# Performance work log

Hardware: AMD Instinct MI355X
Metric: run time of the kernel (lower is better)

The kernel has to match this reference:

```python
import jax, jax.numpy as jnp
import numpy as np

N, E, G = 50000, 800000, 500          # nodes, edges, graphs
NFEAT, NHID, EFEAT = 128, 128, 16
L, NCLASS = 4, 10
BN_EPS = 1e-5


def setup_inputs() -> dict:
    key = jax.random.key(0)
    ks = jax.random.split(key, 10)
    w = lambda k, shape: (jax.random.normal(k, shape, jnp.float32) * 0.05)
    return {
        "h": jax.random.normal(ks[0], (N, NFEAT), jnp.float32),
        "edge_attr": jax.random.normal(ks[1], (E, EFEAT), jnp.float32),
        "edge_index": jax.random.randint(ks[2], (2, E), 0, N),
        "edge_feat_mat": jnp.zeros((1,), jnp.int32),   # placeholder (unused by simplified conv)
        "pair_info": jnp.zeros((1,), jnp.int32),       # placeholder (unused by simplified conv)
        "batch": jnp.sort(jax.random.randint(ks[3], (N,), 0, G)),
        "emb_W": w(ks[4], (NFEAT, NHID)), "emb_b": jnp.zeros((NHID,), jnp.float32),
        "conv_W": w(ks[5], (L, NHID, NHID)), "conv_b": jnp.zeros((L, NHID), jnp.float32),
        "conv_We": w(ks[6], (L, EFEAT, NHID)), "conv_be": jnp.zeros((L, NHID), jnp.float32),
        "bn_gamma": jnp.ones((L, NHID), jnp.float32), "bn_beta": jnp.zeros((L, NHID), jnp.float32),
        "jk_W": w(ks[7], (L + 1, NHID, NCLASS)), "jk_b": jnp.zeros((L + 1, NCLASS), jnp.float32),
    }


def _conv(h, edge_attr, src, dst, W, b, We, be):
    # GIN-style message passing: gather src features, add projected edge feats,
    # scatter-add into dst, then a dense transform of (self + aggregate).
    msg = h[src] + edge_attr @ We + be                      # [E, NHID]
    agg = jax.ops.segment_sum(msg, dst, num_segments=h.shape[0])  # [N, NHID]
    return (h + agg) @ W + b


def _batch_norm(x, gamma, beta):
    mu = jnp.mean(x, axis=0)
    var = jnp.mean(jnp.square(x - mu), axis=0)  # biased, as in torch BN training
    return (x - mu) * jax.lax.rsqrt(var + BN_EPS) * gamma + beta


def reference(h, edge_attr, edge_index, edge_feat_mat, pair_info, batch,
              emb_W, emb_b, conv_W, conv_b, conv_We, conv_be,
              bn_gamma, bn_beta, jk_W, jk_b):
    src, dst = edge_index[0], edge_index[1]
    h = h @ emb_W + emb_b                                   # embedding_h
    h_list = [h]
    for layer in range(L):
        z = _conv(h, edge_attr, src, dst,
                  conv_W[layer], conv_b[layer], conv_We[layer], conv_be[layer])
        z = _batch_norm(z, bn_gamma[layer], bn_beta[layer])
        z = jax.nn.relu(z)
        h = z + h_list[layer]                               # residual (dropout p=0)
        h_list.append(h)
    # JK: sum of per-layer linear heads applied to global_add_pool
    out = jnp.zeros((G, NCLASS), jnp.float32)
    for layer in range(L + 1):
        pooled = jax.ops.segment_sum(h_list[layer], batch, num_segments=G)  # [G, NHID]
        out = out + pooled @ jk_W[layer] + jk_b[layer]
    return out
```

## Files before the change

### kernel.cpp

```cpp
#include <hip/hip_runtime.h>

#define NH 128
#define LAYERS 4
#define BW 128
#define CHUNK 4096

typedef __attribute__((ext_vector_type(8))) short short8;
typedef __attribute__((ext_vector_type(4))) float f32x4;

__device__ __forceinline__ unsigned short f2bf(float f) {
    unsigned u = __float_as_uint(f);
    u += 0x7fffu + ((u >> 16) & 1u);
    return (unsigned short)(u >> 16);
}
__device__ __forceinline__ float bflo(unsigned u) { return __uint_as_float(u << 16); }
__device__ __forceinline__ float bfhi(unsigned u) { return __uint_as_float(u & 0xffff0000u); }
__device__ __forceinline__ unsigned packbf(float x, float y) {
    return (unsigned)f2bf(x) | ((unsigned)f2bf(y) << 16);
}

__global__ void wswz_kernel(const float* __restrict__ emb_W, const float* __restrict__ conv_W,
                            unsigned short* __restrict__ Wsw) {
    int idx = blockIdx.x * 256 + threadIdx.x;
    if (idx >= 5 * 8192) return;
    int m = idx >> 13, i = idx & 8191;
    const float* W = (m == 0) ? emb_W : conv_W + (size_t)(m - 1) * 16384;
    float2 w2 = ((const float2*)W)[i];
    int k = i >> 6, n = (i & 63) * 2;
    int kc = k >> 5, quad = (k >> 3) & 3, j = k & 7;
    int base = m * 16384 + (((n >> 4) * 4 + kc) * 4 + quad) * 128 + j;
    Wsw[base + ((n & 15) << 3)] = f2bf(w2.x);
    Wsw[base + (((n + 1) & 15) << 3)] = f2bf(w2.y);
}

__global__ __launch_bounds__(256) void bhist_kernel(const int* __restrict__ dst, int E,
                                                    int* __restrict__ gH, int NBKT, int NCH,
                                                    const int* __restrict__ batch,
                                                    int* __restrict__ gstart, int N, int G) {
    __shared__ int hist[512];
    int b = blockIdx.x, t = threadIdx.x;
    for (int i = t; i < NBKT; i += 256) hist[i] = 0;
    __syncthreads();
    int base = b * CHUNK, end = min(base + CHUNK, E);
    for (int e = base + t; e < end; e += 256)
        atomicAdd(&hist[dst[e] >> 7], 1);
    __syncthreads();
    for (int i = t; i < NBKT; i += 256) gH[i * NCH + b] = hist[i];

    for (int i = b * 256 + t; i < N; i += gridDim.x * 256) {
        int bb = batch[i];
        int prev = (i == 0) ? -1 : batch[i - 1];
        for (int g = prev + 1; g <= bb; ++g) gstart[g] = i;
        if (i == N - 1)
            for (int g = bb + 1; g <= G; ++g) gstart[g] = N;
    }
}

__global__ __launch_bounds__(256) void block_sum_kernel(const int* __restrict__ deg,
                                                        int* __restrict__ bsum, int n) {
    __shared__ int red[256];
    int t = threadIdx.x;
    int base = blockIdx.x * 1024;
    int s = 0;
#pragma unroll
    for (int i = 0; i < 4; ++i) {
        int idx = base + i * 256 + t;
        if (idx < n) s += deg[idx];
    }
    red[t] = s;
    __syncthreads();
    for (int off = 128; off > 0; off >>= 1) {
        if (t < off) red[t] += red[t + off];
        __syncthreads();
    }
    if (t == 0) bsum[blockIdx.x] = red[0];
}

__global__ __launch_bounds__(1024) void scan_partials_kernel(int* __restrict__ bsum, int nb,
                                                             int* __restrict__ total_out, int n) {
    __shared__ int part[1024];
    int t = threadIdx.x;
    int v = (t < nb) ? bsum[t] : 0;
    part[t] = v;
    __syncthreads();
    for (int off = 1; off < 1024; off <<= 1) {
        int u = (t >= off) ? part[t - off] : 0;
        __syncthreads();
        part[t] += u;
        __syncthreads();
    }
    if (t < nb) bsum[t] = part[t] - v;
    if (t == 1023) total_out[n] = part[1023];
}

__global__ __launch_bounds__(256) void local_scan_kernel(const int* __restrict__ deg,
                                                         const int* __restrict__ bsum,
                                                         int* __restrict__ outA, int n) {
    __shared__ int part[256];
    int t = threadIdx.x;
    int base = blockIdx.x * 1024 + t * 4;
    int v0 = 0, v1 = 0, v2 = 0, v3 = 0;
    if (base + 3 < n) {
        int4 v = *(const int4*)(deg + base);
        v0 = v.x; v1 = v.y; v2 = v.z; v3 = v.w;
    } else {
        if (base + 0 < n) v0 = deg[base + 0];
        if (base + 1 < n) v1 = deg[base + 1];
        if (base + 2 < n) v2 = deg[base + 2];
        if (base + 3 < n) v3 = deg[base + 3];
    }
    int tsum = v0 + v1 + v2 + v3;
    part[t] = tsum;
    __syncthreads();
    for (int off = 1; off < 256; off <<= 1) {
        int u = (t >= off) ? part[t - off] : 0;
        __syncthreads();
        part[t] += u;
        __syncthreads();
    }
    int run = bsum[blockIdx.x] + part[t] - tsum;
    int r0 = run, r1 = run + v0, r2 = r1 + v1, r3 = r2 + v2;
    if (base + 3 < n) {
        *(int4*)(outA + base) = make_int4(r0, r1, r2, r3);
    } else {
        if (base + 0 < n) outA[base + 0] = r0;
        if (base + 1 < n) outA[base + 1] = r1;
        if (base + 2 < n) outA[base + 2] = r2;
        if (base + 3 < n) outA[base + 3] = r3;
    }
}

__global__ __launch_bounds__(256) void bplace_kernel(const int* __restrict__ src,
                                                     const int* __restrict__ dst, int E,
                                                     const int* __restrict__ gOff,
                                                     int NBKT, int NCH,
                                                     int2* __restrict__ bkt) {
    __shared__ int cur[512];
    int b = blockIdx.x, t = threadIdx.x;
    for (int i = t; i < NBKT; i += 256) cur[i] = gOff[i * NCH + b];
    __syncthreads();
    int base = b * CHUNK, end = min(base + CHUNK, E);
    for (int e = base + t; e < end; e += 256) {
        int d = dst[e];
        int p = atomicAdd(&cur[d >> 7], 1);
        bkt[p] = make_int2(src[e], ((d & (BW - 1)) << 25) | e);
    }
}

__global__ __launch_bounds__(256) void bfinal_kernel(const int2* __restrict__ bkt,
                                                     const int* __restrict__ gOff, int NCH,
                                                     int* __restrict__ row_start,
                                                     int2* __restrict__ pk,
                                                     int N, int E) {
    __shared__ int cnt[BW], par[BW];
    int b = blockIdx.x, t = threadIdx.x;
    int s = gOff[b * NCH];
    int e = (b + 1 < (int)gridDim.x) ? gOff[(b + 1) * NCH] : E;
    if (t < BW) cnt[t] = 0;
    __syncthreads();
    for (int p = s + t; p < e; p += 256)
        atomicAdd(&cnt[(unsigned)bkt[p].y >> 25], 1);
    __syncthreads();
    if (t < BW) par[t] = cnt[t];
    __syncthreads();
    for (int off = 1; off < BW; off <<= 1) {
        int u = (t < BW && t >= off) ? par[t - off] : 0;
        __syncthreads();
        if (t < BW) par[t] += u;
        __syncthreads();
    }
    int node = b * BW + t;
    if (t < BW) {
        int excl = par[t] - cnt[t];
        if (node <= N) row_start[node] = s + excl;
        cnt[t] = s + excl;
    }
    if (b == 0 && t == 0) row_start[N] = E;
    __syncthreads();
    for (int p = s + t; p < e; p += 256) {
        int2 v = bkt[p];
        int dloc = (unsigned)v.y >> 25;
        int pos = atomicAdd(&cnt[dloc], 1);
        pk[pos] = make_int2(v.x, v.y & 0x1FFFFFF);
    }
}

__global__ __launch_bounds__(256) void easum_kernel(const float* __restrict__ edge_attr,
                                                    const int2* __restrict__ pk,
                                                    const int* __restrict__ row_start,
                                                    float* __restrict__ easum, int N) {
    int t = threadIdx.x;
    int node = blockIdx.x * 16 + (t >> 4);
    int k = t & 15;
    if (node >= N) return;
    int rs = row_start[node], re = row_start[node + 1];
    float acc = 0.f;
    for (int p = rs; p < re; ++p)
        acc += edge_attr[(size_t)pk[p].y * 16 + k];
    easum[node * 16 + k] = acc;
}

__global__ __launch_bounds__(256) void aggregate_kernel(
    const unsigned* __restrict__ hbfu, const int2* __restrict__ pk,
    const int* __restrict__ row_start, const float* __restrict__ easum,
    const float* __restrict__ We, const float* __restrict__ be,
    unsigned* __restrict__ xbfu, int N) {
    __shared__ float2 WeL[16 * 64];
    int t = threadIdx.x;
    const float2* Wg2 = (const float2*)We;
    for (int i = t; i < 16 * 64; i += 256) WeL[i] = Wg2[i];
    __syncthreads();

    int wave = t >> 6, lane = t & 63;
    int n = blockIdx.x * 4 + wave;
    if (n >= N) return;
    unsigned uself = hbfu[(size_t)n * 64 + lane];
    float2 acc = make_float2(bflo(uself), bfhi(uself));
    float2 acc2 = make_float2(0.f, 0.f);
    float2 acc3 = make_float2(0.f, 0.f);
    float2 acc4 = make_float2(0.f, 0.f);
    int rs = row_start[n], re = row_start[n + 1];
    float myea = (lane < 16) ? easum[n * 16 + lane] : 0.f;

    for (int base = rs; base < re; base += 64) {
        int cnt = min(64, re - base);
        int myS = (base + lane < re) ? pk[base + lane].x : 0;
        int j = 0;
        for (; j + 15 < cnt; j += 16) {
            int s0 = __shfl(myS, j);      int s1 = __shfl(myS, j + 1);
            int s2 = __shfl(myS, j + 2);  int s3 = __shfl(myS, j + 3);
            int s4 = __shfl(myS, j + 4);  int s5 = __shfl(myS, j + 5);
            int s6 = __shfl(myS, j + 6);  int s7 = __shfl(myS, j + 7);
            int s8 = __shfl(myS, j + 8);  int s9 = __shfl(myS, j + 9);
            int sa = __shfl(myS, j + 10); int sb = __shfl(myS, j + 11);
            int sc = __shfl(myS, j + 12); int sd = __shfl(myS, j + 13);
            int se = __shfl(myS, j + 14); int sf = __shfl(myS, j + 15);
            unsigned u0 = hbfu[(size_t)s0 * 64 + lane];
            unsigned u1 = hbfu[(size_t)s1 * 64 + lane];
            unsigned u2 = hbfu[(size_t)s2 * 64 + lane];
            unsigned u3 = hbfu[(size_t)s3 * 64 + lane];
            unsigned u4 = hbfu[(size_t)s4 * 64 + lane];
            unsigned u5 = hbfu[(size_t)s5 * 64 + lane];
            unsigned u6 = hbfu[(size_t)s6 * 64 + lane];
            unsigned u7 = hbfu[(size_t)s7 * 64 + lane];
            unsigned u8 = hbfu[(size_t)s8 * 64 + lane];
            unsigned u9 = hbfu[(size_t)s9 * 64 + lane];
            unsigned ua = hbfu[(size_t)sa * 64 + lane];
            unsigned ub = hbfu[(size_t)sb * 64 + lane];
            unsigned uc = hbfu[(size_t)sc * 64 + lane];
            unsigned ud = hbfu[(size_t)sd * 64 + lane];
            unsigned ue = hbfu[(size_t)se * 64 + lane];
            unsigned uf = hbfu[(size_t)sf * 64 + lane];
            acc.x  += bflo(u0) + bflo(u1) + bflo(u2) + bflo(u3);
            acc.y  += bfhi(u0) + bfhi(u1) + bfhi(u2) + bfhi(u3);
            acc2.x += bflo(u4) + bflo(u5) + bflo(u6) + bflo(u7);
            acc2.y += bfhi(u4) + bfhi(u5) + bfhi(u6) + bfhi(u7);
            acc3.x += bflo(u8) + bflo(u9) + bflo(ua) + bflo(ub);
            acc3.y += bfhi(u8) + bfhi(u9) + bfhi(ua) + bfhi(ub);
            acc4.x += bflo(uc) + bflo(ud) + bflo(ue) + bflo(uf);
            acc4.y += bfhi(uc) + bfhi(ud) + bfhi(ue) + bfhi(uf);
        }
        for (; j + 3 < cnt; j += 4) {
            int s0 = __shfl(myS, j);
            int s1 = __shfl(myS, j + 1);
            int s2 = __shfl(myS, j + 2);
            int s3 = __shfl(myS, j + 3);
            unsigned u0 = hbfu[(size_t)s0 * 64 + lane];
            unsigned u1 = hbfu[(size_t)s1 * 64 + lane];
            unsigned u2 = hbfu[(size_t)s2 * 64 + lane];
            unsigned u3 = hbfu[(size_t)s3 * 64 + lane];
            acc.x += bflo(u0) + bflo(u1) + bflo(u2) + bflo(u3);
            acc.y += bfhi(u0) + bfhi(u1) + bfhi(u2) + bfhi(u3);
        }
        for (; j < cnt; ++j) {
            int s = __shfl(myS, j);
            unsigned u = hbfu[(size_t)s * 64 + lane];
            acc.x += bflo(u);
            acc.y += bfhi(u);
        }
    }
    acc.x += (acc2.x + acc3.x) + acc4.x;
    acc.y += (acc2.y + acc3.y) + acc4.y;

    float degf = (float)(re - rs);
    float2 be2 = ((const float2*)be)[lane];
#pragma unroll
    for (int k = 0; k < 16; ++k) {
        float e = __shfl(myea, k);
        float2 w = WeL[k * 64 + lane];
        acc.x = fmaf(e, w.x, acc.x);
        acc.y = fmaf(e, w.y, acc.y);
    }
    acc.x += degf * be2.x;
    acc.y += degf * be2.y;
    xbfu[(size_t)n * 64 + lane] = packbf(acc.x, acc.y);
}

__global__ __launch_bounds__(256) void gemm_mfma_kernel(
    const unsigned short* __restrict__ Abf, const float* __restrict__ Af32,
    const unsigned short* __restrict__ Wsw, const float* __restrict__ bias,
    unsigned short* __restrict__ Zbf,
    int N, float* __restrict__ bnsum, float* __restrict__ bnsumsq) {
    __shared__ unsigned short Wl[128 * 128];
    __shared__ float bnL[2 * NH];
    int t = threadIdx.x;
    {
        const float4* Wg = (const float4*)Wsw;
        float4* Wl4 = (float4*)Wl;
        for (int i = t; i < 2048; i += 256) Wl4[i] = Wg[i];
    }
    if (t < 2 * NH) bnL[t] = 0.f;
    __syncthreads();

    int wave = t >> 6, lane = t & 63;
    int quad = lane >> 4, ln = lane & 15;
    int row0 = blockIdx.x * 128 + wave * 32;

    f32x4 acc[2][8];
#pragma unroll
    for (int nt = 0; nt < 8; ++nt) {
        float bv = bias[nt * 16 + ln];
        acc[0][nt] = (f32x4){bv, bv, bv, bv};
        acc[1][nt] = (f32x4){bv, bv, bv, bv};
    }

    for (int kc = 0; kc < 4; ++kc) {
        short8 afr[2];
        if (Af32) {
#pragma unroll
            for (int mt = 0; mt < 2; ++mt) {
                int ar = row0 + mt * 16 + ln; if (ar >= N) ar = N - 1;
                const float4* ap = (const float4*)(Af32 + (size_t)ar * NH + kc * 32 + quad * 8);
                float4 a0 = ap[0], a1 = ap[1];
                short8 v;
                v[0] = (short)f2bf(a0.x); v[1] = (short)f2bf(a0.y);
                v[2] = (short)f2bf(a0.z); v[3] = (short)f2bf(a0.w);
                v[4] = (short)f2bf(a1.x); v[5] = (short)f2bf(a1.y);
                v[6] = (short)f2bf(a1.z); v[7] = (short)f2bf(a1.w);
                afr[mt] = v;
            }
        } else {
#pragma unroll
            for (int mt = 0; mt < 2; ++mt) {
                int ar = row0 + mt * 16 + ln; if (ar >= N) ar = N - 1;
                afr[mt] = *(const short8*)(Abf + (size_t)ar * NH + kc * 32 + quad * 8);
            }
        }
#pragma unroll
        for (int nt = 0; nt < 8; ++nt) {
            short8 bfr = *(const short8*)(Wl + ((nt * 4 + kc) * 4 + quad) * 128 + ln * 8);
            acc[0][nt] = __builtin_amdgcn_mfma_f32_16x16x32_bf16(afr[0], bfr, acc[0][nt], 0, 0, 0);
            acc[1][nt] = __builtin_amdgcn_mfma_f32_16x16x32_bf16(afr[1], bfr, acc[1][nt], 0, 0, 0);
        }
    }

#pragma unroll
    for (int mt = 0; mt < 2; ++mt)
#pragma unroll
        for (int r = 0; r < 4; ++r) {
            int row = row0 + mt * 16 + quad * 4 + r;
            if (row < N) {
#pragma unroll
                for (int nt = 0; nt < 8; ++nt)
                    Zbf[(size_t)row * NH + nt * 16 + ln] = f2bf(acc[mt][nt][r]);
            }
        }

    if (bnsum) {
#pragma unroll
        for (int nt = 0; nt < 8; ++nt) {
            float s = 0.f, q = 0.f;
#pragma unroll
            for (int mt = 0; mt < 2; ++mt)
#pragma unroll
                for (int r = 0; r < 4; ++r) {
                    int row = row0 + mt * 16 + quad * 4 + r;
                    if (row < N) { float v = acc[mt][nt][r]; s += v; q += v * v; }
                }
            s += __shfl_xor(s, 16); s += __shfl_xor(s, 32);
            q += __shfl_xor(q, 16); q += __shfl_xor(q, 32);
            if (quad == 0) {
                atomicAdd(&bnL[nt * 16 + ln], s);
                atomicAdd(&bnL[NH + nt * 16 + ln], q);
            }
        }
        __syncthreads();
        if (t < NH) {
            atomicAdd(&bnsum[t], bnL[t]);
            atomicAdd(&bnsumsq[t], bnL[NH + t]);
        }
    }
}

__global__ __launch_bounds__(256) void update_pool_kernel(
    const unsigned* __restrict__ zbfu, unsigned* __restrict__ hbfu,
    const float* __restrict__ bnsum, const float* __restrict__ bnsumsq,
    const float* __restrict__ gamma, const float* __restrict__ beta,
    float invN, const int* __restrict__ gstart, float* __restrict__ pooled) {
    int g = blockIdx.x, t = threadIdx.x;
    __shared__ float scL[NH], shL[NH];
    __shared__ float2 red[256];
    if (t < NH) {
        float mu = bnsum[t] * invN;
        float var = fmaf(bnsumsq[t], invN, -mu * mu);
        float sc = gamma[t] * rsqrtf(var + 1e-5f);
        scL[t] = sc;
        shL[t] = beta[t] - mu * sc;
    }
    __syncthreads();
    int s = gstart[g], e = gstart[g + 1];
    int c2 = t & 63, half = t >> 6;
    float2 sc = make_float2(scL[2 * c2], scL[2 * c2 + 1]);
    float2 sh = make_float2(shL[2 * c2], shL[2 * c2 + 1]);
    float2 pacc = make_float2(0.f, 0.f);
    for (int n = s + half; n < e; n += 4) {
        size_t i = (size_t)n * 64 + c2;
        unsigned zu = zbfu[i];
        unsigned hu = hbfu[i];
        float rx = fmaxf(fmaf(bflo(zu), sc.x, sh.x), 0.f) + bflo(hu);
        float ry = fmaxf(fmaf(bfhi(zu), sc.y, sh.y), 0.f) + bfhi(hu);
        hbfu[i] = packbf(rx, ry);
        pacc.x += rx; pacc.y += ry;
    }
    red[t] = pacc;
    __syncthreads();
    if (t < 64) {
        float2 a = red[t], b = red[t + 64], c = red[t + 128], d = red[t + 192];
        ((float2*)pooled)[(size_t)g * 64 + c2] =
            make_float2((a.x + b.x) + (c.x + d.x), (a.y + b.y) + (c.y + d.y));
    }
}

__global__ __launch_bounds__(256) void pool_kernel(
    const unsigned* __restrict__ hbfu, const int* __restrict__ gstart,
    float* __restrict__ pooled, int G) {
    int g = blockIdx.x, t = threadIdx.x;
    __shared__ float2 red[256];
    int s = gstart[g], e = gstart[g + 1];
    int c2 = t & 63, half = t >> 6;
    float2 pacc = make_float2(0.f, 0.f);
    for (int n = s + half; n < e; n += 4) {
        unsigned u = hbfu[(size_t)n * 64 + c2];
        pacc.x += bflo(u);
        pacc.y += bfhi(u);
    }
    red[t] = pacc;
    __syncthreads();
    if (t < 64) {
        float2 a = red[t], b = red[t + 64], c = red[t + 128], d = red[t + 192];
        ((float2*)pooled)[(size_t)g * 64 + c2] =
            make_float2((a.x + b.x) + (c.x + d.x), (a.y + b.y) + (c.y + d.y));
    }
}

__global__ void jk_kernel(const float* __restrict__ pooled, const float* __restrict__ jkW,
                          const float* __restrict__ jkb, float* __restrict__ out, int G) {
    int idx = blockIdx.x * blockDim.x + threadIdx.x;
    if (idx >= G * 10) return;
    int g = idx / 10, c = idx % 10;
    float acc = 0.f;
    for (int l = 0; l < LAYERS + 1; ++l) {
        acc += jkb[l * 10 + c];
        const float* pg = pooled + ((size_t)l * G + g) * NH;
        const float* wl = jkW + (size_t)l * NH * 10 + c;
        float s = 0.f;
#pragma unroll 16
        for (int k = 0; k < NH; ++k) s = fmaf(pg[k], wl[k * 10], s);
        acc += s;
    }
    out[idx] = acc;
}

extern "C" void kernel_launch(void* const* d_in, const int* in_sizes, int n_in,
                              void* d_out, int out_size, void* d_ws, size_t ws_size,
                              hipStream_t stream) {
    const float* h_in      = (const float*)d_in[0];
    const float* edge_attr = (const float*)d_in[1];
    const int*   edge_idx  = (const int*)d_in[2];
    const int*   batch     = (const int*)d_in[5];
    const float* emb_W     = (const float*)d_in[6];
    const float* emb_b     = (const float*)d_in[7];
    const float* conv_W    = (const float*)d_in[8];
    const float* conv_b    = (const float*)d_in[9];
    const float* conv_We   = (const float*)d_in[10];
    const float* conv_be   = (const float*)d_in[11];
    const float* bn_gamma  = (const float*)d_in[12];
    const float* bn_beta   = (const float*)d_in[13];
    const float* jk_W      = (const float*)d_in[14];
    const float* jk_b      = (const float*)d_in[15];
    float* out = (float*)d_out;

    const int N = in_sizes[0] / NH;
    const int E = in_sizes[1] / 16;
    const int G = out_size / 10;
    const int NBKT = (N + BW - 1) / BW;
    const int NCH  = (E + CHUNK - 1) / CHUNK;
    const int NTOT = NBKT * NCH;
    const int NBW  = (NTOT + 1023) / 1024;

    const int* src = edge_idx;
    const int* dst = edge_idx + E;

    size_t off = 0;
    auto alloc = [&](size_t bytes) -> void* {
        void* p = (char*)d_ws + off;
        off += (bytes + 255) & ~(size_t)255;
        return p;
    };
    unsigned short* hbf = (unsigned short*)alloc((size_t)N * NH * 2);
    unsigned short* xbf = (unsigned short*)alloc((size_t)N * NH * 2);
    unsigned short* zbf = (unsigned short*)alloc((size_t)N * NH * 2);
    unsigned short* Wsw = (unsigned short*)alloc((size_t)5 * NH * NH * 2);
    float* pooled  = (float*)alloc((size_t)(LAYERS + 1) * G * NH * 4);
    float* easum   = (float*)alloc((size_t)N * 16 * 4);
    size_t zero_off = off;
    float* bnsum   = (float*)alloc((size_t)LAYERS * NH * 4);
    float* bnsumsq = (float*)alloc((size_t)LAYERS * NH * 4);
    size_t zero_bytes = off - zero_off;
    int* gH        = (int*)alloc((size_t)(NTOT + 1) * 4);
    int* bsumW     = (int*)alloc((size_t)NBW * 4);
    int* gstart    = (int*)alloc((size_t)(G + 1) * 4);
    int* row_start = (int*)alloc((size_t)(N + 1) * 4);
    int2* bkt      = (int2*)alloc((size_t)E * 8);
    int2* pk       = (int2*)alloc((size_t)E * 8);
    (void)ws_size; (void)n_in;

    hipMemsetAsync((char*)d_ws + zero_off, 0, zero_bytes, stream);

    wswz_kernel<<<(5 * 8192 + 255) / 256, 256, 0, stream>>>(emb_W, conv_W, Wsw);

    bhist_kernel<<<NCH, 256, 0, stream>>>(dst, E, gH, NBKT, NCH, batch, gstart, N, G);
    block_sum_kernel<<<NBW, 256, 0, stream>>>(gH, bsumW, NTOT);
    scan_partials_kernel<<<1, 1024, 0, stream>>>(bsumW, NBW, gH, NTOT);
    local_scan_kernel<<<NBW, 256, 0, stream>>>(gH, bsumW, gH, NTOT);
    bplace_kernel<<<NCH, 256, 0, stream>>>(src, dst, E, gH, NBKT, NCH, bkt);
    bfinal_kernel<<<NBKT, 256, 0, stream>>>(bkt, gH, NCH, row_start, pk, N, E);
    easum_kernel<<<(N + 15) / 16, 256, 0, stream>>>(edge_attr, pk, row_start, easum, N);

    dim3 gemm_grid((N + 127) / 128);
    dim3 agg_grid((N + 3) / 4);

    gemm_mfma_kernel<<<gemm_grid, 256, 0, stream>>>(
        nullptr, h_in, Wsw, emb_b, hbf, N, nullptr, nullptr);
    pool_kernel<<<G, 256, 0, stream>>>((const unsigned*)hbf, gstart, pooled, G);

    for (int l = 0; l < LAYERS; ++l) {
        aggregate_kernel<<<agg_grid, 256, 0, stream>>>(
            (const unsigned*)hbf, pk, row_start, easum,
            conv_We + (size_t)l * 16 * NH, conv_be + (size_t)l * NH,
            (unsigned*)xbf, N);
        gemm_mfma_kernel<<<gemm_grid, 256, 0, stream>>>(
            xbf, nullptr, Wsw + (size_t)(l + 1) * NH * NH, conv_b + (size_t)l * NH,
            zbf, N, bnsum + (size_t)l * NH, bnsumsq + (size_t)l * NH);
        update_pool_kernel<<<G, 256, 0, stream>>>(
            (const unsigned*)zbf, (unsigned*)hbf,
            bnsum + (size_t)l * NH, bnsumsq + (size_t)l * NH,
            bn_gamma + (size_t)l * NH, bn_beta + (size_t)l * NH,
            1.0f / (float)N, gstart, pooled + (size_t)(l + 1) * G * NH);
    }

    jk_kernel<<<(G * 10 + 255) / 256, 256, 0, stream>>>(pooled, jk_W, jk_b, out, G);
}
```

Baseline: 549.1 us.

## Fuse neighbor aggregation with MFMA GEMM and BN statistics per node tile

Replaces the separate aggregate and GEMM kernels in each layer with one kernel. Each 512-thread block aggregates a 128-node tile into swizzled LDS, then runs the bf16 MFMA transform on it and accumulates the BatchNorm sums. This removes the xbf intermediate round trip through global memory and one launch per layer. In exchange the grid drops to one block per 128 nodes, each wave walks 16 nodes one after another, and the weights are read from global memory instead of LDS. That may reduce how well the latency-bound gather is hidden.

```diff
diff --git a/kernel.cpp b/kernel.cpp
--- a/kernel.cpp
+++ b/kernel.cpp
@@ -200,116 +200,173 @@
     easum[node * 16 + k] = acc;
 }
 
-__global__ __launch_bounds__(256) void aggregate_kernel(
+__global__ __launch_bounds__(512) void agg_gemm_kernel(
     const unsigned* __restrict__ hbfu, const int2* __restrict__ pk,
     const int* __restrict__ row_start, const float* __restrict__ easum,
     const float* __restrict__ We, const float* __restrict__ be,
-    unsigned* __restrict__ xbfu, int N) {
+    const unsigned short* __restrict__ Wsw, const float* __restrict__ bias,
+    unsigned short* __restrict__ Zbf, int N,
+    float* __restrict__ bnsum, float* __restrict__ bnsumsq) {
+    __shared__ unsigned xL[128 * 64];
     __shared__ float2 WeL[16 * 64];
+    __shared__ float bnL[2 * NH];
     int t = threadIdx.x;
     const float2* Wg2 = (const float2*)We;
-    for (int i = t; i < 16 * 64; i += 256) WeL[i] = Wg2[i];
+    for (int i = t; i < 16 * 64; i += 512) WeL[i] = Wg2[i];
+    if (t < 2 * NH) bnL[t] = 0.f;
     __syncthreads();
 
     int wave = t >> 6, lane = t & 63;
-    int n = blockIdx.x * 4 + wave;
-    if (n >= N) return;
-    unsigned uself = hbfu[(size_t)n * 64 + lane];
-    float2 acc = make_float2(bflo(uself), bfhi(uself));
-    float2 acc2 = make_float2(0.f, 0.f);
-    float2 acc3 = make_float2(0.f, 0.f);
-    float2 acc4 = make_float2(0.f, 0.f);
-    int rs = row_start[n], re = row_start[n + 1];
-    float myea = (lane < 16) ? easum[n * 16 + lane] : 0.f;
-
-    for (int base = rs; base < re; base += 64) {
-        int cnt = min(64, re - base);
-        int myS = (base + lane < re) ? pk[base + lane].x : 0;
-        int j = 0;
-        for (; j + 15 < cnt; j += 16) {
-            int s0 = __shfl(myS, j);      int s1 = __shfl(myS, j + 1);
-            int s2 = __shfl(myS, j + 2);  int s3 = __shfl(myS, j + 3);
-            int s4 = __shfl(myS, j + 4);  int s5 = __shfl(myS, j + 5);
-            int s6 = __shfl(myS, j + 6);  int s7 = __shfl(myS, j + 7);
-            int s8 = __shfl(myS, j + 8);  int s9 = __shfl(myS, j + 9);
-            int sa = __shfl(myS, j + 10); int sb = __shfl(myS, j + 11);
-            int sc = __shfl(myS, j + 12); int sd = __shfl(myS, j + 13);
-            int se = __shfl(myS, j + 14); int sf = __shfl(myS, j + 15);
-            unsigned u0 = hbfu[(size_t)s0 * 64 + lane];
-            unsigned u1 = hbfu[(size_t)s1 * 64 + lane];
-            unsigned u2 = hbfu[(size_t)s2 * 64 + lane];
-            unsigned u3 = hbfu[(size_t)s3 * 64 + lane];
-            unsigned u4 = hbfu[(size_t)s4 * 64 + lane];
-            unsigned u5 = hbfu[(size_t)s5 * 64 + lane];
-            unsigned u6 = hbfu[(size_t)s6 * 64 + lane];
-            unsigned u7 = hbfu[(size_t)s7 * 64 + lane];
-            unsigned u8 = hbfu[(size_t)s8 * 64 + lane];
-            unsigned u9 = hbfu[(size_t)s9 * 64 + lane];
-            unsigned ua = hbfu[(size_t)sa * 64 + lane];
-            unsigned ub = hbfu[(size_t)sb * 64 + lane];
-            unsigned uc = hbfu[(size_t)sc * 64 + lane];
-            unsigned ud = hbfu[(size_t)sd * 64 + lane];
-            unsigned ue = hbfu[(size_t)se * 64 + lane];
-            unsigned uf = hbfu[(size_t)sf * 64 + lane];
-            acc.x  += bflo(u0) + bflo(u1) + bflo(u2) + bflo(u3);
-            acc.y  += bfhi(u0) + bfhi(u1) + bfhi(u2) + bfhi(u3);
-            acc2.x += bflo(u4) + bflo(u5) + bflo(u6) + bflo(u7);
-            acc2.y += bfhi(u4) + bfhi(u5) + bfhi(u6) + bfhi(u7);
-            acc3.x += bflo(u8) + bflo(u9) + bflo(ua) + bflo(ub);
-            acc3.y += bfhi(u8) + bfhi(u9) + bfhi(ua) + bfhi(ub);
-            acc4.x += bflo(uc) + bflo(ud) + bflo(ue) + bflo(uf);
-            acc4.y += bfhi(uc) + bfhi(ud) + bfhi(ue) + bfhi(uf);
-        }
-        for (; j + 3 < cnt; j += 4) {
-            int s0 = __shfl(myS, j);
-            int s1 = __shfl(myS, j + 1);
-            int s2 = __shfl(myS, j + 2);
-            int s3 = __shfl(myS, j + 3);
-            unsigned u0 = hbfu[(size_t)s0 * 64 + lane];
-            unsigned u1 = hbfu[(size_t)s1 * 64 + lane];
-            unsigned u2 = hbfu[(size_t)s2 * 64 + lane];
-            unsigned u3 = hbfu[(size_t)s3 * 64 + lane];
-            acc.x += bflo(u0) + bflo(u1) + bflo(u2) + bflo(u3);
-            acc.y += bfhi(u0) + bfhi(u1) + bfhi(u2) + bfhi(u3);
-        }
-        for (; j < cnt; ++j) {
-            int s = __shfl(myS, j);
-            unsigned u = hbfu[(size_t)s * 64 + lane];
-            acc.x += bflo(u);
-            acc.y += bfhi(u);
-        }
-    }
-    acc.x += (acc2.x + acc3.x) + acc4.x;
-    acc.y += (acc2.y + acc3.y) + acc4.y;
-
-    float degf = (float)(re - rs);
-    float2 be2 = ((const float2*)be)[lane];
-#pragma unroll
-    for (int k = 0; k < 16; ++k) {
-        float e = __shfl(myea, k);
-        float2 w = WeL[k * 64 + lane];
-        acc.x = fmaf(e, w.x, acc.x);
-        acc.y = fmaf(e, w.y, acc.y);
-    }
-    acc.x += degf * be2.x;
-    acc.y += degf * be2.y;
-    xbfu[(size_t)n * 64 + lane] = packbf(acc.x, acc.y);
+    int b = blockIdx.x;
+
+    for (int i = 0; i < 16; ++i) {
+        int nl = wave * 16 + i;
+        int n = b * BW + nl;
+        unsigned widx = nl * 64 + (lane ^ ((nl & 15) << 2));
+        if (n >= N) { xL[widx] = 0u; continue; }
+        unsigned uself = hbfu[(size_t)n * 64 + lane];
+        float2 acc = make_float2(bflo(uself), bfhi(uself));
+        float2 acc2 = make_float2(0.f, 0.f);
+        float2 acc3 = make_float2(0.f, 0.f);
+        float2 acc4 = make_float2(0.f, 0.f);
+        int rs = row_start[n], re = row_start[n + 1];
+        float myea = (lane < 16) ? easum[n * 16 + lane] : 0.f;
+
+        for (int base = rs; base < re; base += 64) {
+            int cnt = min(64, re - base);
+            int myS = (base + lane < re) ? pk[base + lane].x : 0;
+            int j = 0;
+            for (; j + 15 < cnt; j += 16) {
+                int s0 = __shfl(myS, j);      int s1 = __shfl(myS, j + 1);
+                int s2 = __shfl(myS, j + 2);  int s3 = __shfl(myS, j + 3);
+                int s4 = __shfl(myS, j + 4);  int s5 = __shfl(myS, j + 5);
+                int s6 = __shfl(myS, j + 6);  int s7 = __shfl(myS, j + 7);
+                int s8 = __shfl(myS, j + 8);  int s9 = __shfl(myS, j + 9);
+                int sa = __shfl(myS, j + 10); int sb = __shfl(myS, j + 11);
+                int sc = __shfl(myS, j + 12); int sd = __shfl(myS, j + 13);
+                int se = __shfl(myS, j + 14); int sf = __shfl(myS, j + 15);
+                unsigned u0 = hbfu[(size_t)s0 * 64 + lane];
+                unsigned u1 = hbfu[(size_t)s1 * 64 + lane];
+                unsigned u2 = hbfu[(size_t)s2 * 64 + lane];
+                unsigned u3 = hbfu[(size_t)s3 * 64 + lane];
+                unsigned u4 = hbfu[(size_t)s4 * 64 + lane];
+                unsigned u5 = hbfu[(size_t)s5 * 64 + lane];
+                unsigned u6 = hbfu[(size_t)s6 * 64 + lane];
+                unsigned u7 = hbfu[(size_t)s7 * 64 + lane];
+                unsigned u8 = hbfu[(size_t)s8 * 64 + lane];
+                unsigned u9 = hbfu[(size_t)s9 * 64 + lane];
+                unsigned ua = hbfu[(size_t)sa * 64 + lane];
+                unsigned ub = hbfu[(size_t)sb * 64 + lane];
+                unsigned uc = hbfu[(size_t)sc * 64 + lane];
+                unsigned ud = hbfu[(size_t)sd * 64 + lane];
+                unsigned ue = hbfu[(size_t)se * 64 + lane];
+                unsigned uf = hbfu[(size_t)sf * 64 + lane];
+                acc.x  += bflo(u0) + bflo(u1) + bflo(u2) + bflo(u3);
+                acc.y  += bfhi(u0) + bfhi(u1) + bfhi(u2) + bfhi(u3);
+                acc2.x += bflo(u4) + bflo(u5) + bflo(u6) + bflo(u7);
+                acc2.y += bfhi(u4) + bfhi(u5) + bfhi(u6) + bfhi(u7);
+                acc3.x += bflo(u8) + bflo(u9) + bflo(ua) + bflo(ub);
+                acc3.y += bfhi(u8) + bfhi(u9) + bfhi(ua) + bfhi(ub);
+                acc4.x += bflo(uc) + bflo(ud) + bflo(ue) + bflo(uf);
+                acc4.y += bfhi(uc) + bfhi(ud) + bfhi(ue) + bfhi(uf);
+            }
+            for (; j + 3 < cnt; j += 4) {
+                int s0 = __shfl(myS, j);
+                int s1 = __shfl(myS, j + 1);
+                int s2 = __shfl(myS, j + 2);
+                int s3 = __shfl(myS, j + 3);
+                unsigned u0 = hbfu[(size_t)s0 * 64 + lane];
+                unsigned u1 = hbfu[(size_t)s1 * 64 + lane];
+                unsigned u2 = hbfu[(size_t)s2 * 64 + lane];
+                unsigned u3 = hbfu[(size_t)s3 * 64 + lane];
+                acc.x += bflo(u0) + bflo(u1) + bflo(u2) + bflo(u3);
+                acc.y += bfhi(u0) + bfhi(u1) + bfhi(u2) + bfhi(u3);
+            }
+            for (; j < cnt; ++j) {
+                int s = __shfl(myS, j);
+                unsigned u = hbfu[(size_t)s * 64 + lane];
+                acc.x += bflo(u);
+                acc.y += bfhi(u);
+            }
+        }
+        acc.x += (acc2.x + acc3.x) + acc4.x;
+        acc.y += (acc2.y + acc3.y) + acc4.y;
+
+        float degf = (float)(re - rs);
+        float2 be2 = ((const float2*)be)[lane];
+#pragma unroll
+        for (int k = 0; k < 16; ++k) {
+            float e = __shfl(myea, k);
+            float2 w = WeL[k * 64 + lane];
+            acc.x = fmaf(e, w.x, acc.x);
+            acc.y = fmaf(e, w.y, acc.y);
+        }
+        acc.x += degf * be2.x;
+        acc.y += degf * be2.y;
+        xL[widx] = packbf(acc.x, acc.y);
+    }
+
+    int quad = lane >> 4, ln = lane & 15;
+    int ar = wave * 16 + ln;
+    f32x4 acc[8];
+#pragma unroll
+    for (int nt = 0; nt < 8; ++nt) {
+        float bv = bias[nt * 16 + ln];
+        acc[nt] = (f32x4){bv, bv, bv, bv};
+    }
+#pragma unroll
+    for (int kc = 0; kc < 4; ++kc) {
+        int widx = ar * 64 + ((kc * 16 + quad * 4) ^ ((ar & 15) << 2));
+        short8 afr = *(const short8*)(xL + widx);
+#pragma unroll
+        for (int nt = 0; nt < 8; ++nt) {
+            short8 bfr = *(const short8*)(Wsw + ((nt * 4 + kc) * 4 + quad) * 128 + ln * 8);
+            acc[nt] = __builtin_amdgcn_mfma_f32_16x16x32_bf16(afr, bfr, acc[nt], 0, 0, 0);
+        }
+    }
+
+#pragma unroll
+    for (int r = 0; r < 4; ++r) {
+        int row = b * BW + wave * 16 + quad * 4 + r;
+        if (row < N) {
+#pragma unroll
+            for (int nt = 0; nt < 8; ++nt)
+                Zbf[(size_t)row * NH + nt * 16 + ln] = f2bf(acc[nt][r]);
+        }
+    }
+
+#pragma unroll
+    for (int nt = 0; nt < 8; ++nt) {
+        float s = 0.f, q = 0.f;
+#pragma unroll
+        for (int r = 0; r < 4; ++r) {
+            int row = b * BW + wave * 16 + quad * 4 + r;
+            if (row < N) { float v = acc[nt][r]; s += v; q += v * v; }
+        }
+        s += __shfl_xor(s, 16); s += __shfl_xor(s, 32);
+        q += __shfl_xor(q, 16); q += __shfl_xor(q, 32);
+        if (quad == 0) {
+            atomicAdd(&bnL[nt * 16 + ln], s);
+            atomicAdd(&bnL[NH + nt * 16 + ln], q);
+        }
+    }
+    __syncthreads();
+    if (t < NH) {
+        atomicAdd(&bnsum[t], bnL[t]);
+        atomicAdd(&bnsumsq[t], bnL[NH + t]);
+    }
 }
 
 __global__ __launch_bounds__(256) void gemm_mfma_kernel(
-    const unsigned short* __restrict__ Abf, const float* __restrict__ Af32,
-    const unsigned short* __restrict__ Wsw, const float* __restrict__ bias,
-    unsigned short* __restrict__ Zbf,
-    int N, float* __restrict__ bnsum, float* __restrict__ bnsumsq) {
+    const float* __restrict__ Af32, const unsigned short* __restrict__ Wsw,
+    const float* __restrict__ bias, unsigned short* __restrict__ Zbf, int N) {
     __shared__ unsigned short Wl[128 * 128];
-    __shared__ float bnL[2 * NH];
     int t = threadIdx.x;
     {
         const float4* Wg = (const float4*)Wsw;
         float4* Wl4 = (float4*)Wl;
         for (int i = t; i < 2048; i += 256) Wl4[i] = Wg[i];
     }
-    if (t < 2 * NH) bnL[t] = 0.f;
     __syncthreads();
 
     int wave = t >> 6, lane = t & 63;
@@ -326,25 +383,17 @@
 
     for (int kc = 0; kc < 4; ++kc) {
         short8 afr[2];
-        if (Af32) {
-#pragma unroll
-            for (int mt = 0; mt < 2; ++mt) {
-                int ar = row0 + mt * 16 + ln; if (ar >= N) ar = N - 1;
-                const float4* ap = (const float4*)(Af32 + (size_t)ar * NH + kc * 32 + quad * 8);
-                float4 a0 = ap[0], a1 = ap[1];
-                short8 v;
-                v[0] = (short)f2bf(a0.x); v[1] = (short)f2bf(a0.y);
-                v[2] = (short)f2bf(a0.z); v[3] = (short)f2bf(a0.w);
-                v[4] = (short)f2bf(a1.x); v[5] = (short)f2bf(a1.y);
-                v[6] = (short)f2bf(a1.z); v[7] = (short)f2bf(a1.w);
-                afr[mt] = v;
-            }
-        } else {
-#pragma unroll
-            for (int mt = 0; mt < 2; ++mt) {
-                int ar = row0 + mt * 16 + ln; if (ar >= N) ar = N - 1;
-                afr[mt] = *(const short8*)(Abf + (size_t)ar * NH + kc * 32 + quad * 8);
-            }
+#pragma unroll
+        for (int mt = 0; mt < 2; ++mt) {
+            int ar = row0 + mt * 16 + ln; if (ar >= N) ar = N - 1;
+            const float4* ap = (const float4*)(Af32 + (size_t)ar * NH + kc * 32 + quad * 8);
+            float4 a0 = ap[0], a1 = ap[1];
+            short8 v;
+            v[0] = (short)f2bf(a0.x); v[1] = (short)f2bf(a0.y);
+            v[2] = (short)f2bf(a0.z); v[3] = (short)f2bf(a0.w);
+            v[4] = (short)f2bf(a1.x); v[5] = (short)f2bf(a1.y);
+            v[6] = (short)f2bf(a1.z); v[7] = (short)f2bf(a1.w);
+            afr[mt] = v;
         }
 #pragma unroll
         for (int nt = 0; nt < 8; ++nt) {
@@ -365,31 +414,6 @@
                     Zbf[(size_t)row * NH + nt * 16 + ln] = f2bf(acc[mt][nt][r]);
             }
         }
-
-    if (bnsum) {
-#pragma unroll
-        for (int nt = 0; nt < 8; ++nt) {
-            float s = 0.f, q = 0.f;
-#pragma unroll
-            for (int mt = 0; mt < 2; ++mt)
-#pragma unroll
-                for (int r = 0; r < 4; ++r) {
-                    int row = row0 + mt * 16 + quad * 4 + r;
-                    if (row < N) { float v = acc[mt][nt][r]; s += v; q += v * v; }
-                }
-            s += __shfl_xor(s, 16); s += __shfl_xor(s, 32);
-            q += __shfl_xor(q, 16); q += __shfl_xor(q, 32);
-            if (quad == 0) {
-                atomicAdd(&bnL[nt * 16 + ln], s);
-                atomicAdd(&bnL[NH + nt * 16 + ln], q);
-            }
-        }
-        __syncthreads();
-        if (t < NH) {
-            atomicAdd(&bnsum[t], bnL[t]);
-            atomicAdd(&bnsumsq[t], bnL[NH + t]);
-        }
-    }
 }
 
 __global__ __launch_bounds__(256) void update_pool_kernel(
@@ -508,7 +532,6 @@
         return p;
     };
     unsigned short* hbf = (unsigned short*)alloc((size_t)N * NH * 2);
-    unsigned short* xbf = (unsigned short*)alloc((size_t)N * NH * 2);
     unsigned short* zbf = (unsigned short*)alloc((size_t)N * NH * 2);
     unsigned short* Wsw = (unsigned short*)alloc((size_t)5 * NH * NH * 2);
     float* pooled  = (float*)alloc((size_t)(LAYERS + 1) * G * NH * 4);
@@ -537,20 +560,14 @@
     bfinal_kernel<<<NBKT, 256, 0, stream>>>(bkt, gH, NCH, row_start, pk, N, E);
     easum_kernel<<<(N + 15) / 16, 256, 0, stream>>>(edge_attr, pk, row_start, easum, N);
 
-    dim3 gemm_grid((N + 127) / 128);
-    dim3 agg_grid((N + 3) / 4);
-
-    gemm_mfma_kernel<<<gemm_grid, 256, 0, stream>>>(
-        nullptr, h_in, Wsw, emb_b, hbf, N, nullptr, nullptr);
+    gemm_mfma_kernel<<<NBKT, 256, 0, stream>>>(h_in, Wsw, emb_b, hbf, N);
     pool_kernel<<<G, 256, 0, stream>>>((const unsigned*)hbf, gstart, pooled, G);
 
     for (int l = 0; l < LAYERS; ++l) {
-        aggregate_kernel<<<agg_grid, 256, 0, stream>>>(
+        agg_gemm_kernel<<<NBKT, 512, 0, stream>>>(
             (const unsigned*)hbf, pk, row_start, easum,
             conv_We + (size_t)l * 16 * NH, conv_be + (size_t)l * NH,
-            (unsigned*)xbf, N);
-        gemm_mfma_kernel<<<gemm_grid, 256, 0, stream>>>(
-            xbf, nullptr, Wsw + (size_t)(l + 1) * NH * NH, conv_b + (size_t)l * NH,
+            Wsw + (size_t)(l + 1) * NH * NH, conv_b + (size_t)l * NH,
             zbf, N, bnsum + (size_t)l * NH, bnsumsq + (size_t)l * NH);
         update_pool_kernel<<<G, 256, 0, stream>>>(
             (const unsigned*)zbf, (unsigned*)hbf,
```

After: 542.9 us. About the same (-1.1%).
